# Kernel optimization log

Measured on AMD Instinct MI355X. Metric: run time of the kernel, lower is better.

The kernel has to match this reference:

```python
import jax, jax.numpy as jnp
from jax import lax
import numpy as np

B, S, N, F, H = 8, 32, 1024, 4, 128

def setup_inputs() -> dict:
    key = jax.random.key(0)
    ks = jax.random.split(key, 8)
    x = jax.random.normal(ks[0], (B, S, N, F), dtype=jnp.float32)
    # normalized-Laplacian-like dense adjacency (register_buffer in torch)
    adj = jax.random.uniform(ks[1], (N, N), dtype=jnp.float32) / N
    sc1 = 1.0 / np.sqrt(H + F)
    W1 = jax.random.normal(ks[2], (H + F, 3 * H), dtype=jnp.float32) * sc1
    b1 = jnp.ones((3 * H,), dtype=jnp.float32)  # bias init 1.0
    W2 = jax.random.normal(ks[3], (H + F, H), dtype=jnp.float32) * sc1
    b2 = jnp.zeros((H,), dtype=jnp.float32)
    scl = 1.0 / np.sqrt(H)
    W_ih = jax.random.normal(ks[4], (4 * H, H), dtype=jnp.float32) * scl
    W_hh = jax.random.normal(ks[5], (4 * H, H), dtype=jnp.float32) * scl
    b_ih = jnp.zeros((4 * H,), dtype=jnp.float32)
    b_hh = jnp.zeros((4 * H,), dtype=jnp.float32)
    return {"x": x, "adj": adj, "W1": W1, "b1": b1, "W2": W2, "b2": b2,
            "W_ih": W_ih, "W_hh": W_hh, "b_ih": b_ih, "b_hh": b_hh}


def reference(x, adj, W1, b1, W2, b2, W_ih, W_hh, b_ih, b_hh):
    b, s, n, f = x.shape
    h = W2.shape[1]

    def gconv(inp, hid, W, bb):
        # inp: (B,N,F), hid flat: (B, N*H)
        cat = jnp.concatenate([inp, hid.reshape(b, n, h)], axis=2)  # (B,N,F+H)
        ac = jnp.einsum('mn,bnc->bmc', adj, cat)                    # Laplacian @ feats
        out = ac @ W + bb                                           # (B,N,out_dim)
        return out.reshape(b, -1)

    def enc_step(carry, inp):
        hid, cell = carry
        conc = jax.nn.sigmoid(gconv(inp, hid, W1, b1))  # (B, N*3H)
        fg, ig, og = jnp.split(conc, 3, axis=1)         # chunk over flattened dim (as torch)
        cs = jnp.tanh(gconv(inp, hid, W2, b2))          # (B, N*H)
        cnew = fg * cell + ig * cs
        hnew = og * jnp.tanh(cnew)
        # NB: original returns the OLD cell_state (bug preserved)
        return (hnew, cell), hnew.reshape(b, n, h)

    x_t = jnp.transpose(x, (1, 0, 2, 3))  # (S,B,N,F)
    zeros_bnh = jnp.zeros((b, n * h), x.dtype)
    (_, _), hseq = lax.scan(enc_step, (zeros_bnh, zeros_bnh), x_t)  # (S,B,N,H)

    hseq = jnp.transpose(hseq.reshape(s, b * n, h), (1, 0, 2))  # (B*N, S, H)

    def att_step(carry, _):
        hx, cx = carry
        e = jnp.einsum('bsh,bh->bs', hseq, hx)[..., None]  # (BN,S,1)
        scores = jax.nn.softmax(e, axis=-1)                # softmax over size-1 axis (as torch)
        ctx = (hseq * scores).sum(1)                       # (BN,H)
        gates = ctx @ W_ih.T + b_ih + hx @ W_hh.T + b_hh   # (BN,4H)
        ig, fg, gg, og = jnp.split(gates, 4, axis=1)
        cxn = jax.nn.sigmoid(fg) * cx + jax.nn.sigmoid(ig) * jnp.tanh(gg)
        hxn = jax.nn.sigmoid(og) * jnp.tanh(cxn)
        return (hxn, cxn), None

    hx0 = jnp.zeros((n * b, h), x.dtype)
    (hx, _), _ = lax.scan(att_step, (hx0, hx0), None, length=s)
    return hx.reshape(b, n, h)
```

## Files before the change

kernel.cpp:

```cpp
#include <hip/hip_runtime.h>
#include <hip/hip_bf16.h>

#define B_   8
#define S_   32
#define N_   1024
#define H_   128
#define NH_  131072u

typedef float f32;
typedef _Float16 f16;
typedef _Float16 half8 __attribute__((ext_vector_type(8)));
typedef float f32x4 __attribute__((ext_vector_type(4)));
typedef float f32x16 __attribute__((ext_vector_type(16)));

__device__ __forceinline__ float sig_fast(float x){
    return __builtin_amdgcn_rcpf(1.0f + __expf(-x));
}
__device__ __forceinline__ float tanh_fast(float x){
    return 1.0f - 2.0f*__builtin_amdgcn_rcpf(1.0f + __expf(2.0f*x));
}

__global__ void kzero(f32* __restrict__ p, int n){
    int i = blockIdx.x*blockDim.x + threadIdx.x;
    int stride = gridDim.x*blockDim.x;
    for(; i<n; i+=stride) p[i] = 0.f;
}

__global__ void kprep(const f32* __restrict__ adj,
                      const f32* __restrict__ W1, const f32* __restrict__ b1,
                      const f32* __restrict__ W2, const f32* __restrict__ b2,
                      const f32* __restrict__ Wih, const f32* __restrict__ Whh,
                      const f32* __restrict__ bih, const f32* __restrict__ bhh,
                      f16* __restrict__ adj16, f16* __restrict__ WzX16,
                      f16* __restrict__ Whh16, f32* __restrict__ WihT,
                      f32* __restrict__ bias512, f32* __restrict__ biasP)
{
    int i = blockIdx.x*blockDim.x + threadIdx.x;
    if(i < 1048576) adj16[i] = (f16)adj[i];
    if(i < 81920){
        int j = i/160, k = i - j*160;
        float v;
        if(k < 128)      v = (j<384) ? W1[(4+k)*384 + j] : W2[(4+k)*128 + (j-384)];
        else if(k < 132) v = (j<384) ? W1[(k-128)*384 + j] : W2[(k-128)*128 + (j-384)];
        else             v = 0.f;
        WzX16[i] = (f16)v;
    }
    if(i < 65536){
        Whh16[i] = (f16)Whh[i];
        int k = i>>9, jj = i&511;
        WihT[i] = Wih[jj*128 + k];
    }
    if(i < 512){
        bias512[i] = (i<384) ? b1[i] : b2[i-384];
        biasP[i]   = bih[i] + bhh[i];
    }
}

__global__ void ktransx(const f32* __restrict__ x, f16* __restrict__ XrT){
    int o = blockIdx.x*blockDim.x + threadIdx.x;
    int m = o & 1023, q = o >> 10;
    int f = q & 3, b = (q>>2)&7, t = q>>5;
    XrT[o] = (f16)x[((b*32+t)<<12) + (m<<2) + f];
}

__global__ __launch_bounds__(256, 4)
void kbigAXP(const f16* __restrict__ A, const f16* __restrict__ Bt, f16* __restrict__ C)
{
    const int lane = threadIdx.x & 63;
    const int w = threadIdx.x >> 6;
    const int row0 = blockIdx.y*32, col0 = blockIdx.x*32;

    const int mr = row0 + (lane & 31);
    const int nc = col0 + (lane & 31);
    const int kb = w*256 + (lane>>5)*8;
    const f16* Ap = A  + (size_t)mr*1024 + kb;
    const f16* Bp = Bt + (size_t)nc*1024 + kb;

    half8 Ab[8], Bb[8];
    #pragma unroll
    for(int i=0;i<8;i++){
        Ab[i] = *(const half8*)(Ap + i*16);
        Bb[i] = *(const half8*)(Bp + i*16);
    }
    f32x16 acc0 = {}, acc1 = {};
    #pragma unroll
    for(int it=0; it<16; ++it){
        half8 av = Ab[it&7], bv = Bb[it&7];
        if(it < 8){
            Ab[it] = *(const half8*)(Ap + (it+8)*16);
            Bb[it] = *(const half8*)(Bp + (it+8)*16);
        }
        if(it & 1) acc1 = __builtin_amdgcn_mfma_f32_32x32x16_f16(av, bv, acc1, 0,0,0);
        else       acc0 = __builtin_amdgcn_mfma_f32_32x32x16_f16(av, bv, acc0, 0,0,0);
    }
    f32x16 acc = acc0 + acc1;

    __shared__ float red[3][32][32];
    if(w > 0){
        #pragma unroll
        for(int i=0;i<16;i++){
            int r = (i&3) + 8*(i>>2) + 4*(lane>>5);
            red[w-1][r][lane&31] = acc[i];
        }
    }
    __syncthreads();
    if(w == 0){
        #pragma unroll
        for(int i=0;i<16;i++){
            int r = (i&3) + 8*(i>>2) + 4*(lane>>5);
            int c = lane & 31;
            float v = acc[i] + red[0][r][c] + red[1][r][c] + red[2][r][c];
            C[(size_t)(row0 + r)*1024 + col0 + c] = (f16)v;
        }
    }
}

__global__ __launch_bounds__(512)
void kfz(const f16* __restrict__ adj16, const f16* __restrict__ hidT,
         const f16* __restrict__ WzX16, const f16* __restrict__ AXP16,
         const f32* __restrict__ bias512, f32* __restrict__ act, int t)
{
    const int tid = threadIdx.x;
    const int lane = tid & 63;
    const int w = tid >> 6;
    const int q = w & 3, kh = w >> 2;
    const int b = blockIdx.x;
    const int m0 = blockIdx.y * 32;

    __shared__ float red[4][32][32];
    __shared__ f16 Zs[32][160];

    {
        const int mr = m0 + (lane & 31);
        const int nc = b*128 + q*32 + (lane & 31);
        const int kb = kh*512 + (lane>>5)*8;
        const f16* Ap = adj16 + (size_t)mr*1024 + kb;
        const f16* Bp = hidT  + (size_t)nc*1024 + kb;

        half8 Ab[8], Bb[8];
        #pragma unroll
        for(int i=0;i<8;i++){
            Ab[i] = *(const half8*)(Ap + i*16);
            Bb[i] = *(const half8*)(Bp + i*16);
        }
        f32x16 acc0 = {}, acc1 = {};
        #pragma unroll
        for(int it=0; it<32; ++it){
            half8 av = Ab[it&7], bv = Bb[it&7];
            if(it < 24){
                Ab[it&7] = *(const half8*)(Ap + (it+8)*16);
                Bb[it&7] = *(const half8*)(Bp + (it+8)*16);
            }
            if(it & 1) acc1 = __builtin_amdgcn_mfma_f32_32x32x16_f16(av, bv, acc1, 0,0,0);
            else       acc0 = __builtin_amdgcn_mfma_f32_32x32x16_f16(av, bv, acc0, 0,0,0);
        }
        f32x16 acc = acc0 + acc1;

        if(kh == 1){
            #pragma unroll
            for(int i=0;i<16;i++){
                int r = (i&3) + 8*(i>>2) + 4*(lane>>5);
                red[q][r][lane&31] = acc[i];
            }
            int local = tid & 255;
            if(local < 128){
                int m = local>>2, f = local&3;
                Zs[m][128+f] = AXP16[(size_t)(m0+m)*1024 + t*32 + b*4 + f];
            }
            for(int idx = local; idx < 32*28; idx += 256){
                int r = idx/28, c = 132 + idx - r*28;
                Zs[r][c] = (f16)0.f;
            }
        }
        __syncthreads();
        if(kh == 0){
            #pragma unroll
            for(int i=0;i<16;i++){
                int r = (i&3) + 8*(i>>2) + 4*(lane>>5);
                int c = lane & 31;
                Zs[r][q*32 + c] = (f16)(acc[i] + red[q][r][c]);
            }
        }
        __syncthreads();
    }

    const int lr = lane & 15, kc = lane >> 4;
    const int cbase = w*64;
    const f16* Bp2 = WzX16 + (size_t)(cbase + lr)*160 + kc*8;

    f32x4 acc2[2][4] = {};
    #pragma unroll
    for(int k0=0; k0<160; k0+=32){
        half8 a0 = *(const half8*)&Zs[lr][kc*8 + k0];
        half8 a1 = *(const half8*)&Zs[16+lr][kc*8 + k0];
        #pragma unroll
        for(int f=0; f<4; f++){
            half8 bb = *(const half8*)(Bp2 + (size_t)f*16*160 + k0);
            acc2[0][f] = __builtin_amdgcn_mfma_f32_16x16x32_f16(a0, bb, acc2[0][f], 0,0,0);
            acc2[1][f] = __builtin_amdgcn_mfma_f32_16x16x32_f16(a1, bb, acc2[1][f], 0,0,0);
        }
    }
    #pragma unroll
    for(int a=0;a<2;a++)
      #pragma unroll
      for(int f=0; f<4; f++)
        #pragma unroll
        for(int i=0; i<4; i++){
            int m = m0 + a*16 + kc*4 + i;
            int j = cbase + f*16 + lr;
            float v = acc2[a][f][i] + bias512[j];
            act[(size_t)(m*8+b)*512 + j] = (j<384) ? sig_fast(v) : tanh_fast(v);
        }
}

__global__ void kscr(const f32* __restrict__ act, f16* __restrict__ hidT,
                     f32* __restrict__ ctx)
{
    int blk = blockIdx.x;
    int b  = blk >> 6;
    int n0 = (blk & 63) * 16;
    __shared__ f16 th[16][128];
    #pragma unroll
    for(int i=0;i<8;i++){
        int flat = i*256 + threadIdx.x;
        int nl = flat >> 7, c = flat & 127;
        int n = n0 + nl;
        int p = n*128 + c;
        unsigned q1 = (unsigned)p + NH_, q2 = (unsigned)p + 2u*NH_;
        unsigned n1 = q1/384u, j1 = q1 - n1*384u;
        unsigned n2 = q2/384u, j2 = q2 - n2*384u;
        float ig = act[(size_t)(n1*8u + b)*512u + j1];
        float og = act[(size_t)(n2*8u + b)*512u + j2];
        float cs = act[(size_t)((unsigned)n*8u + b)*512u + 384u + c];
        float h = og * tanh_fast(ig*cs);
        ctx[((b<<10)|n)*128 + c] += h;
        th[nl][c] = (f16)h;
    }
    __syncthreads();
    int c_o = threadIdx.x >> 1, half = threadIdx.x & 1;
    half8 v;
    #pragma unroll
    for(int j=0;j<8;j++) v[j] = th[half*8+j][c_o];
    *(half8*)(hidT + (size_t)(b*128 + c_o)*1024 + n0 + half*8) = v;
}

__global__ __launch_bounds__(256)
void gemmCtxA(const f32* __restrict__ A, const f32* __restrict__ Bm, f32* __restrict__ C,
              const f32* __restrict__ bias)
{
    __shared__ float As[16][68];
    __shared__ float Bs[16][64];
    const int tid = threadIdx.x;
    const int tx = tid & 15, ty = tid >> 4;
    const int col0 = blockIdx.x*64, row0 = blockIdx.y*64;
    const int am = tid >> 2, aq = tid & 3;
    const int bcol = tid & 63, bkr = tid >> 6;
    const int lda = 128, ldb = 512, Ncol = 512, K = 128;

    float acc[4][4] = {};
    for(int k0 = 0; k0 < K; k0 += 16){
        const float4 a4 = *(const float4*)(A + (size_t)(row0+am)*lda + k0 + aq*4);
        float bv[4];
        #pragma unroll
        for(int i=0;i<4;i++) bv[i] = Bm[(size_t)(k0 + bkr*4 + i)*ldb + col0 + bcol];
        #pragma unroll
        for(int i=0;i<4;i++) As[aq*4+i][am] = ((const float*)&a4)[i];
        #pragma unroll
        for(int i=0;i<4;i++) Bs[bkr*4+i][bcol] = bv[i];
        __syncthreads();
        #pragma unroll
        for(int kk=0;kk<16;kk++){
            float4 av  = *(const float4*)&As[kk][ty*4];
            float4 bvv = *(const float4*)&Bs[kk][tx*4];
            #pragma unroll
            for(int i=0;i<4;i++)
                #pragma unroll
                for(int j=0;j<4;j++)
                    acc[i][j] += ((const float*)&av)[i] * ((const float*)&bvv)[j];
        }
        __syncthreads();
    }
    #pragma unroll
    for(int i=0;i<4;i++){
        int r = row0 + ty*4 + i;
        #pragma unroll
        for(int j=0;j<4;j++){
            int cidx = col0 + tx*4 + j;
            C[(size_t)r*Ncol + cidx] = acc[i][j] + bias[cidx];
        }
    }
}

__global__ __launch_bounds__(512)
void kdec(const f16* __restrict__ Whh16, const f32* __restrict__ ctxA,
          f32* __restrict__ out)
{
    const int lane = threadIdx.x & 63;
    const int w = threadIdx.x >> 6;
    const int r0 = blockIdx.x * 32;
    const int lr = lane & 15, kc = lane >> 4;
    const int cw = w*16 + lr;

    __shared__ f16 hx[32][152];
    {
        f16* hp = &hx[0][0];
        for(int i = threadIdx.x; i < 32*152; i += 512) hp[i] = (f16)0.f;
    }

    half8 wreg[4][4];
    #pragma unroll
    for(int kk=0; kk<4; ++kk)
      #pragma unroll
      for(int g=0; g<4; ++g)
        wreg[kk][g] = *(const half8*)(Whh16 + (size_t)(g*128 + cw)*128 + kc*8 + kk*32);

    float ca[2][4][4];
    float cxr[2][4];
    #pragma unroll
    for(int a=0;a<2;a++)
      #pragma unroll
      for(int i=0;i<4;i++){
        int r = r0 + a*16 + kc*4 + i;
        #pragma unroll
        for(int g=0;g<4;g++)
            ca[a][g][i] = ctxA[(size_t)r*512 + g*128 + cw];
        cxr[a][i] = 0.f;
      }
    __syncthreads();

    for(int s=0; s<32; ++s){
        f32x4 acc[2][4] = {};
        #pragma unroll
        for(int kk=0; kk<4; ++kk){
            half8 a0 = *(const half8*)&hx[lr][kc*8 + kk*32];
            half8 a1 = *(const half8*)&hx[16+lr][kc*8 + kk*32];
            #pragma unroll
            for(int g=0; g<4; ++g){
                acc[0][g] = __builtin_amdgcn_mfma_f32_16x16x32_f16(a0, wreg[kk][g], acc[0][g], 0,0,0);
                acc[1][g] = __builtin_amdgcn_mfma_f32_16x16x32_f16(a1, wreg[kk][g], acc[1][g], 0,0,0);
            }
        }
        __syncthreads();
        #pragma unroll
        for(int a=0;a<2;a++)
          #pragma unroll
          for(int i=0;i<4;i++){
            float ig = sig_fast (acc[a][0][i] + ca[a][0][i]);
            float fg = sig_fast (acc[a][1][i] + ca[a][1][i]);
            float gg = tanh_fast(acc[a][2][i] + ca[a][2][i]);
            float og = sig_fast (acc[a][3][i] + ca[a][3][i]);
            float cv = fg*cxr[a][i] + ig*gg;
            cxr[a][i] = cv;
            float h = og*tanh_fast(cv);
            int rloc = a*16 + kc*4 + i;
            hx[rloc][cw] = (f16)h;
            if(s==31) out[(size_t)(r0 + rloc)*128 + cw] = h;
          }
        __syncthreads();
    }
}

extern "C" void kernel_launch(void* const* d_in, const int* in_sizes, int n_in,
                              void* d_out, int out_size, void* d_ws, size_t ws_size,
                              hipStream_t stream) {
    const f32* x   = (const f32*)d_in[0];
    const f32* adj = (const f32*)d_in[1];
    const f32* W1  = (const f32*)d_in[2];
    const f32* b1  = (const f32*)d_in[3];
    const f32* W2  = (const f32*)d_in[4];
    const f32* b2  = (const f32*)d_in[5];
    const f32* Wih = (const f32*)d_in[6];
    const f32* Whh = (const f32*)d_in[7];
    const f32* bih = (const f32*)d_in[8];
    const f32* bhh = (const f32*)d_in[9];
    f32* out = (f32*)d_out;
    f32* ws  = (f32*)d_ws;

    f32* ctx    = ws;
    f16* hidT   = (f16*)(ws + 1048576);
    f32* act    = ws + 2228224;
    f32* ctxA   = ws + 6422528;
    f16* AXP16  = (f16*)(ws + 10616832);
    f16* XrT    = (f16*)(ws + 11141120);
    f16* adj16  = (f16*)(ws + 11665408);
    f16* WzX16  = (f16*)(ws + 12189696);
    f16* Whh16  = (f16*)(ws + 12230656);
    f32* WihT   = ws + 12263424;
    f32* bias512= ws + 12328960;
    f32* biasP  = ws + 12329472;

    const int TPB = 256;
    hipLaunchKernelGGL(kzero, dim3(2048), dim3(TPB), 0, stream, ws, 1572864);
    hipLaunchKernelGGL(kprep, dim3(4096), dim3(TPB), 0, stream,
                       adj, W1,b1,W2,b2, Wih,Whh,bih,bhh,
                       adj16, WzX16, Whh16, WihT, bias512, biasP);
    hipLaunchKernelGGL(ktransx, dim3(4096), dim3(TPB), 0, stream, x, XrT);

    hipLaunchKernelGGL(kbigAXP, dim3(32,32), dim3(TPB), 0, stream, adj16, XrT, AXP16);

    for(int t = 0; t < S_; ++t){
        hipLaunchKernelGGL(kfz, dim3(8,32), dim3(512), 0, stream,
                           adj16, hidT, WzX16, AXP16, bias512, act, t);
        hipLaunchKernelGGL(kscr, dim3(512), dim3(TPB), 0, stream, act, hidT, ctx);
    }

    hipLaunchKernelGGL(gemmCtxA, dim3(8,128), dim3(TPB), 0, stream, ctx, WihT, ctxA, biasP);

    hipLaunchKernelGGL(kdec, dim3(256), dim3(512), 0, stream, Whh16, ctxA, out);
}
```

Baseline: 1.091 ms.

## Fuse gate GEMM and state update into one per-step kernel with recomputed chunk rows

Merges the per-timestep gate kernel and the elementwise cell-update kernel into a single kstep kernel. Because of the flattened chunk split, each block's forget/input/output gates come from other nodes' rows. The block therefore also computes the 16 extra adjacency rows it needs for the input and output gates and keeps all gate pre-activations in shared memory. This removes the large act buffer round trip through global memory and one launch per step. At t=0 it skips the adjacency GEMM because the hidden state is zero, and it overwrites ctx instead of accumulating, which makes the zeroing kernel unnecessary. In exchange it does about twice the adjacency GEMM work per block and drops the K-split across waves, so each wave runs a longer serial MFMA chain.

```diff
diff --git a/kernel.cpp b/kernel.cpp
--- a/kernel.cpp
+++ b/kernel.cpp
@@ -18,12 +18,6 @@
 }
 __device__ __forceinline__ float tanh_fast(float x){
     return 1.0f - 2.0f*__builtin_amdgcn_rcpf(1.0f + __expf(2.0f*x));
-}
-
-__global__ void kzero(f32* __restrict__ p, int n){
-    int i = blockIdx.x*blockDim.x + threadIdx.x;
-    int stride = gridDim.x*blockDim.x;
-    for(; i<n; i+=stride) p[i] = 0.f;
 }
 
 __global__ void kprep(const f32* __restrict__ adj,
@@ -116,26 +110,31 @@
 }
 
 __global__ __launch_bounds__(512)
-void kfz(const f16* __restrict__ adj16, const f16* __restrict__ hidT,
-         const f16* __restrict__ WzX16, const f16* __restrict__ AXP16,
-         const f32* __restrict__ bias512, f32* __restrict__ act, int t)
+void kstep(const f16* __restrict__ adj16, const f16* __restrict__ WzX16,
+           const f16* __restrict__ AXP16, const f32* __restrict__ bias512,
+           f16* __restrict__ hidT, f32* __restrict__ ctx, int t)
 {
     const int tid = threadIdx.x;
     const int lane = tid & 63;
     const int w = tid >> 6;
-    const int q = w & 3, kh = w >> 2;
-    const int b = blockIdx.x;
-    const int m0 = blockIdx.y * 32;
-
-    __shared__ float red[4][32][32];
-    __shared__ f16 Zs[32][160];
-
-    {
-        const int mr = m0 + (lane & 31);
-        const int nc = b*128 + q*32 + (lane & 31);
-        const int kb = kh*512 + (lane>>5)*8;
-        const f16* Ap = adj16 + (size_t)mr*1024 + kb;
-        const f16* Bp = hidT  + (size_t)nc*1024 + kb;
+    const int b = blockIdx.x & 7;
+    const int m0 = (blockIdx.x >> 3) * 32;
+    const int igBase = (int)((NH_  + (unsigned)m0*128u)/384u);
+    const int ogBase = (int)((2u*NH_ + (unsigned)m0*128u)/384u);
+
+    __shared__ f16 Zs[64][168];
+    __shared__ f32 aP2[32][128];
+    __shared__ f32 aIG[16][384];
+    __shared__ f32 aOG[16][384];
+    __shared__ f16 th[32][136];
+
+    if(t > 0){
+        const int rt = w >> 2, cq = w & 3;
+        const int r = rt*32 + (lane & 31);
+        int node = (r < 32) ? (m0 + r) : ((r < 48) ? (igBase + r - 32) : (ogBase + r - 48));
+        if(node > 1023) node = 1023;
+        const f16* Ap = adj16 + (size_t)node*1024 + (lane>>5)*8;
+        const f16* Bp = hidT  + (size_t)(b*128 + cq*32 + (lane&31))*1024 + (lane>>5)*8;
 
         half8 Ab[8], Bb[8];
         #pragma unroll
@@ -145,9 +144,9 @@
         }
         f32x16 acc0 = {}, acc1 = {};
         #pragma unroll
-        for(int it=0; it<32; ++it){
+        for(int it=0; it<64; ++it){
             half8 av = Ab[it&7], bv = Bb[it&7];
-            if(it < 24){
+            if(it < 56){
                 Ab[it&7] = *(const half8*)(Ap + (it+8)*16);
                 Bb[it&7] = *(const half8*)(Bp + (it+8)*16);
             }
@@ -155,93 +154,84 @@
             else       acc0 = __builtin_amdgcn_mfma_f32_32x32x16_f16(av, bv, acc0, 0,0,0);
         }
         f32x16 acc = acc0 + acc1;
-
-        if(kh == 1){
+        #pragma unroll
+        for(int i=0;i<16;i++){
+            int rr = (i&3) + 8*(i>>2) + 4*(lane>>5);
+            Zs[rt*32 + rr][cq*32 + (lane&31)] = (f16)acc[i];
+        }
+    } else {
+        #pragma unroll
+        for(int it=0; it<16; ++it){
+            int flat = it*512 + tid;
+            Zs[flat>>7][flat&127] = (f16)0.f;
+        }
+    }
+    if(tid < 256){
+        int r = tid >> 2, f = tid & 3;
+        int node = (r < 32) ? (m0 + r) : ((r < 48) ? (igBase + r - 32) : (ogBase + r - 48));
+        if(node > 1023) node = 1023;
+        Zs[r][128+f] = AXP16[(size_t)node*1024 + t*32 + b*4 + f];
+    }
+    for(int idx = tid; idx < 64*28; idx += 512){
+        int r = idx/28, c2 = 132 + (idx - r*28);
+        Zs[r][c2] = (f16)0.f;
+    }
+    __syncthreads();
+
+    {
+        int rbase, jbase; f32* dst; int dstride;
+        if(w < 2){      rbase = w*16; jbase = 384;       dst = &aP2[w*16][0]; dstride = 128; }
+        else if(w < 5){ rbase = 32;   jbase = (w-2)*128; dst = &aIG[0][0] + jbase; dstride = 384; }
+        else {          rbase = 48;   jbase = (w-5)*128; dst = &aOG[0][0] + jbase; dstride = 384; }
+        const int lr = lane & 15, kc = lane >> 4;
+        const f16* Ap2 = &Zs[rbase + lr][kc*8];
+        const f16* Bp2 = WzX16 + (size_t)(jbase + lr)*160 + kc*8;
+
+        f32x4 acc[8] = {};
+        #pragma unroll
+        for(int k0=0; k0<160; k0+=32){
+            half8 a = *(const half8*)(Ap2 + k0);
             #pragma unroll
-            for(int i=0;i<16;i++){
-                int r = (i&3) + 8*(i>>2) + 4*(lane>>5);
-                red[q][r][lane&31] = acc[i];
+            for(int f=0; f<8; f++){
+                half8 bb = *(const half8*)(Bp2 + (size_t)f*16*160 + k0);
+                acc[f] = __builtin_amdgcn_mfma_f32_16x16x32_f16(a, bb, acc[f], 0,0,0);
             }
-            int local = tid & 255;
-            if(local < 128){
-                int m = local>>2, f = local&3;
-                Zs[m][128+f] = AXP16[(size_t)(m0+m)*1024 + t*32 + b*4 + f];
-            }
-            for(int idx = local; idx < 32*28; idx += 256){
-                int r = idx/28, c = 132 + idx - r*28;
-                Zs[r][c] = (f16)0.f;
-            }
-        }
-        __syncthreads();
-        if(kh == 0){
-            #pragma unroll
-            for(int i=0;i<16;i++){
-                int r = (i&3) + 8*(i>>2) + 4*(lane>>5);
-                int c = lane & 31;
-                Zs[r][q*32 + c] = (f16)(acc[i] + red[q][r][c]);
-            }
-        }
-        __syncthreads();
-    }
-
-    const int lr = lane & 15, kc = lane >> 4;
-    const int cbase = w*64;
-    const f16* Bp2 = WzX16 + (size_t)(cbase + lr)*160 + kc*8;
-
-    f32x4 acc2[2][4] = {};
-    #pragma unroll
-    for(int k0=0; k0<160; k0+=32){
-        half8 a0 = *(const half8*)&Zs[lr][kc*8 + k0];
-        half8 a1 = *(const half8*)&Zs[16+lr][kc*8 + k0];
-        #pragma unroll
-        for(int f=0; f<4; f++){
-            half8 bb = *(const half8*)(Bp2 + (size_t)f*16*160 + k0);
-            acc2[0][f] = __builtin_amdgcn_mfma_f32_16x16x32_f16(a0, bb, acc2[0][f], 0,0,0);
-            acc2[1][f] = __builtin_amdgcn_mfma_f32_16x16x32_f16(a1, bb, acc2[1][f], 0,0,0);
-        }
-    }
-    #pragma unroll
-    for(int a=0;a<2;a++)
-      #pragma unroll
-      for(int f=0; f<4; f++)
-        #pragma unroll
-        for(int i=0; i<4; i++){
-            int m = m0 + a*16 + kc*4 + i;
-            int j = cbase + f*16 + lr;
-            float v = acc2[a][f][i] + bias512[j];
-            act[(size_t)(m*8+b)*512 + j] = (j<384) ? sig_fast(v) : tanh_fast(v);
-        }
-}
-
-__global__ void kscr(const f32* __restrict__ act, f16* __restrict__ hidT,
-                     f32* __restrict__ ctx)
-{
-    int blk = blockIdx.x;
-    int b  = blk >> 6;
-    int n0 = (blk & 63) * 16;
-    __shared__ f16 th[16][128];
-    #pragma unroll
-    for(int i=0;i<8;i++){
-        int flat = i*256 + threadIdx.x;
+        }
+        #pragma unroll
+        for(int f=0; f<8; f++)
+          #pragma unroll
+          for(int i=0; i<4; i++){
+            int rl = kc*4 + i;
+            int col = f*16 + lr;
+            dst[rl*dstride + col] = acc[f][i] + bias512[jbase + col];
+          }
+    }
+    __syncthreads();
+
+    #pragma unroll
+    for(int it=0; it<8; ++it){
+        int flat = it*512 + tid;
         int nl = flat >> 7, c = flat & 127;
-        int n = n0 + nl;
-        int p = n*128 + c;
-        unsigned q1 = (unsigned)p + NH_, q2 = (unsigned)p + 2u*NH_;
+        unsigned p = (unsigned)((m0 + nl)*128 + c);
+        unsigned q1 = p + NH_, q2 = p + 2u*NH_;
         unsigned n1 = q1/384u, j1 = q1 - n1*384u;
         unsigned n2 = q2/384u, j2 = q2 - n2*384u;
-        float ig = act[(size_t)(n1*8u + b)*512u + j1];
-        float og = act[(size_t)(n2*8u + b)*512u + j2];
-        float cs = act[(size_t)((unsigned)n*8u + b)*512u + 384u + c];
-        float h = og * tanh_fast(ig*cs);
-        ctx[((b<<10)|n)*128 + c] += h;
+        float igv = sig_fast(aIG[(int)n1 - igBase][j1]);
+        float ogv = sig_fast(aOG[(int)n2 - ogBase][j2]);
+        float cs  = tanh_fast(aP2[nl][c]);
+        float h = ogv * tanh_fast(igv * cs);
+        size_t ci = (size_t)(((b<<10) | (m0 + nl))*128 + c);
+        if(t == 0) ctx[ci] = h; else ctx[ci] += h;
         th[nl][c] = (f16)h;
     }
     __syncthreads();
-    int c_o = threadIdx.x >> 1, half = threadIdx.x & 1;
-    half8 v;
-    #pragma unroll
-    for(int j=0;j<8;j++) v[j] = th[half*8+j][c_o];
-    *(half8*)(hidT + (size_t)(b*128 + c_o)*1024 + n0 + half*8) = v;
+    {
+        int c_o = tid >> 2, oct = tid & 3;
+        half8 v;
+        #pragma unroll
+        for(int j=0;j<8;j++) v[j] = th[oct*8+j][c_o];
+        *(half8*)(hidT + (size_t)(b*128 + c_o)*1024 + m0 + oct*8) = v;
+    }
 }
 
 __global__ __launch_bounds__(256)
@@ -378,7 +368,6 @@
 
     f32* ctx    = ws;
     f16* hidT   = (f16*)(ws + 1048576);
-    f32* act    = ws + 2228224;
     f32* ctxA   = ws + 6422528;
     f16* AXP16  = (f16*)(ws + 10616832);
     f16* XrT    = (f16*)(ws + 11141120);
@@ -390,7 +379,6 @@
     f32* biasP  = ws + 12329472;
 
     const int TPB = 256;
-    hipLaunchKernelGGL(kzero, dim3(2048), dim3(TPB), 0, stream, ws, 1572864);
     hipLaunchKernelGGL(kprep, dim3(4096), dim3(TPB), 0, stream,
                        adj, W1,b1,W2,b2, Wih,Whh,bih,bhh,
                        adj16, WzX16, Whh16, WihT, bias512, biasP);
@@ -399,9 +387,8 @@
     hipLaunchKernelGGL(kbigAXP, dim3(32,32), dim3(TPB), 0, stream, adj16, XrT, AXP16);
 
     for(int t = 0; t < S_; ++t){
-        hipLaunchKernelGGL(kfz, dim3(8,32), dim3(512), 0, stream,
-                           adj16, hidT, WzX16, AXP16, bias512, act, t);
-        hipLaunchKernelGGL(kscr, dim3(512), dim3(TPB), 0, stream, act, hidT, ctx);
+        hipLaunchKernelGGL(kstep, dim3(256), dim3(512), 0, stream,
+                           adj16, WzX16, AXP16, bias512, hidT, ctx, t);
     }
 
     hipLaunchKernelGGL(gemmCtxA, dim3(8,128), dim3(TPB), 0, stream, ctx, WihT, ctxA, biasP);
```

Result: slower. 1.296 ms (+18.7%).
